# Optimization experiments

Hardware: AMD Instinct MI355X
Metric: run time of the kernel (lower is better)

The kernel has to match this reference:

```python
import jax, jax.numpy as jnp
import numpy as np
from jax import lax

BETA = 0.95
THR = 1.0
NUM_STEPS = 25
BATCH = 262144
NUM_IN, NUM_HID, NUM_OUT = 9, 100, 2


@jax.custom_vjp
def spike(u):
    # Heaviside step with ATan surrogate gradient (snntorch default, alpha=2.0)
    return (u > 0).astype(u.dtype)

def _spike_fwd(u):
    return spike(u), u

def _spike_bwd(u, g):
    return (g / (1.0 + (jnp.pi * u) ** 2),)

spike.defvjp(_spike_fwd, _spike_bwd)


def setup_inputs() -> dict:
    key = jax.random.key(0)
    k1, k2, k3, k4, k5 = jax.random.split(key, 5)
    x = jax.random.uniform(k1, (BATCH, NUM_IN), dtype=jnp.float32)
    # PyTorch-style uniform init scale ~1/sqrt(fan_in), scaled normals are fine
    W1 = jax.random.normal(k2, (NUM_HID, NUM_IN), dtype=jnp.float32) / np.sqrt(NUM_IN)
    b1 = jax.random.normal(k3, (NUM_HID,), dtype=jnp.float32) / np.sqrt(NUM_IN)
    W2 = jax.random.normal(k4, (NUM_OUT, NUM_HID), dtype=jnp.float32) / np.sqrt(NUM_HID)
    b2 = jax.random.normal(k5, (NUM_OUT,), dtype=jnp.float32) / np.sqrt(NUM_HID)
    return {"x": x, "W1": W1, "b1": b1, "W2": W2, "b2": b2}


def reference(x, W1, b1, W2, b2):
    # cur1 is identical every step (input x is static), compute once
    cur1 = x @ W1.T + b1  # [B, H]
    mem1_0 = jnp.zeros((x.shape[0], NUM_HID), dtype=x.dtype)
    mem2_0 = jnp.zeros((x.shape[0], NUM_OUT), dtype=x.dtype)

    def step(carry, _):
        mem1, mem2 = carry
        # snntorch Leaky (reset_mechanism='subtract'):
        #   reset is spike of the OLD membrane, detached from the graph
        reset1 = lax.stop_gradient(spike(mem1 - THR))
        mem1 = BETA * mem1 + cur1 - reset1 * THR
        spk1 = spike(mem1 - THR)
        cur2 = spk1 @ W2.T + b2  # [B, O]
        reset2 = lax.stop_gradient(spike(mem2 - THR))
        mem2 = BETA * mem2 + cur2 - reset2 * THR
        spk2 = spike(mem2 - THR)
        return (mem1, mem2), (spk2, mem2)

    _, (spk2_rec, mem2_rec) = lax.scan(step, (mem1_0, mem2_0), None, length=NUM_STEPS)
    return spk2_rec, mem2_rec  # each [T, B, O]
```

## Files before the change

### kernel.cpp

```cpp
#include <hip/hip_runtime.h>

#define BATCH 262144
#define NI 9
#define NH 100
#define NO 2
#define T 25


typedef float f32x2 __attribute__((ext_vector_type(2)));

#define TSTEP(t) \
  "v_pk_fma_f32 v[8:9], v[4:5], v[8:9], v[10:11]\n\t"                          \
  "v_pk_fma_f32 v[8:9], v[12:13], v[0:1], v[8:9]\n\t"                          \
  "v_pk_fma_f32 v[14:15], v[6:7], v[8:9], v[2:3]\n\t"                          \
  "v_med3_f32 v12, v14, 0, 1.0\n\t"                                            \
  "v_med3_f32 v13, v15, 0, 1.0\n\t"                                            \
  "v_pk_fma_f32 %[a" #t "], v[16:17], v[12:13], %[a" #t "] op_sel:[0,0,0] op_sel_hi:[1,0,1]\n\t" \
  "v_pk_fma_f32 %[a" #t "], v[18:19], v[12:13], %[a" #t "] op_sel:[0,1,0] op_sel_hi:[1,1,1]\n\t"

__global__
__attribute__((amdgpu_flat_work_group_size(256, 256), amdgpu_waves_per_eu(4, 8)))
void snn_fwd(
    const float* __restrict__ x,
    const float* __restrict__ W1,
    const float* __restrict__ b1,
    const float* __restrict__ W2,
    const float* __restrict__ b2,
    float* __restrict__ out)
{
    __shared__ f32x2 red[13 * 128];

    const int tid  = threadIdx.x;
    const int lane = tid & 63;
    const int w    = tid >> 6;
    const int half = __builtin_amdgcn_readfirstlane(w & 1);
    const int el   = (w >> 1) * 64 + lane;
    const int e    = blockIdx.x * 128 + el;

    float xi[NI];
#pragma unroll
    for (int i = 0; i < NI; ++i) xi[i] = x[(size_t)e * NI + i];

    f32x2 acc[T];
#pragma unroll
    for (int t = 0; t < T; ++t) { acc[t].x = 0.0f; acc[t].y = 0.0f; }

    const float* W1h = W1 + half * 50 * NI;
    const float* b1h = b1 + half * 50;
    const float* W2h = W2 + half * 50;

    asm volatile(
        "s_mov_b64 s[40:41], %[pw1]\n\t"
        "s_mov_b64 s[42:43], %[pb1]\n\t"
        "s_mov_b64 s[44:45], %[pw2]\n\t"
        "v_mov_b32 v0, 0xbf800000\n\t"
        "v_mov_b32 v1, 0xbf800000\n\t"
        "v_mov_b32 v2, 0xdd800000\n\t"
        "v_mov_b32 v3, 0xdd800000\n\t"
        "v_mov_b32 v4, 0x3f733333\n\t"
        "v_mov_b32 v5, 0x3f733333\n\t"
        "v_mov_b32 v6, 0x5d800000\n\t"
        "v_mov_b32 v7, 0x5d800000\n\t"
        "s_mov_b32 s46, 25\n\t"
        "s_load_dwordx16 s[48:63], s[40:41], 0x0\n\t"
        "s_load_dwordx2 s[64:65], s[40:41], 0x40\n\t"
        "s_load_dwordx2 s[66:67], s[42:43], 0x0\n\t"
        "s_load_dword s68, s[44:45], 0x0\n\t"
        "s_load_dword s69, s[44:45], 0x190\n\t"
        "s_load_dword s70, s[44:45], 0x4\n\t"
        "s_load_dword s71, s[44:45], 0x194\n\t"
        "1:\n\t"
        "s_waitcnt lgkmcnt(0)\n\t"
        "v_mov_b32 v16, s68\n\t"
        "v_mov_b32 v17, s69\n\t"
        "v_mov_b32 v18, s70\n\t"
        "v_mov_b32 v19, s71\n\t"
        "v_mul_f32 v10, s48, %[x0]\n\t"
        "v_fma_f32 v10, s49, %[x1], v10\n\t"
        "v_fma_f32 v10, s50, %[x2], v10\n\t"
        "v_fma_f32 v10, s51, %[x3], v10\n\t"
        "v_fma_f32 v10, s52, %[x4], v10\n\t"
        "v_fma_f32 v10, s53, %[x5], v10\n\t"
        "v_fma_f32 v10, s54, %[x6], v10\n\t"
        "v_fma_f32 v10, s55, %[x7], v10\n\t"
        "v_fma_f32 v10, s56, %[x8], v10\n\t"
        "v_add_f32 v10, s66, v10\n\t"
        "v_mul_f32 v11, s57, %[x0]\n\t"
        "v_fma_f32 v11, s58, %[x1], v11\n\t"
        "v_fma_f32 v11, s59, %[x2], v11\n\t"
        "v_fma_f32 v11, s60, %[x3], v11\n\t"
        "v_fma_f32 v11, s61, %[x4], v11\n\t"
        "v_fma_f32 v11, s62, %[x5], v11\n\t"
        "v_fma_f32 v11, s63, %[x6], v11\n\t"
        "v_fma_f32 v11, s64, %[x7], v11\n\t"
        "v_fma_f32 v11, s65, %[x8], v11\n\t"
        "v_add_f32 v11, s67, v11\n\t"
        "s_cmp_lg_u32 s46, 1\n\t"
        "s_cbranch_scc0 2f\n\t"
        "s_add_u32 s40, s40, 72\n\t"
        "s_addc_u32 s41, s41, 0\n\t"
        "s_add_u32 s42, s42, 8\n\t"
        "s_addc_u32 s43, s43, 0\n\t"
        "s_add_u32 s44, s44, 8\n\t"
        "s_addc_u32 s45, s45, 0\n\t"
        "s_load_dwordx16 s[48:63], s[40:41], 0x0\n\t"
        "s_load_dwordx2 s[64:65], s[40:41], 0x40\n\t"
        "s_load_dwordx2 s[66:67], s[42:43], 0x0\n\t"
        "s_load_dword s68, s[44:45], 0x0\n\t"
        "s_load_dword s69, s[44:45], 0x190\n\t"
        "s_load_dword s70, s[44:45], 0x4\n\t"
        "s_load_dword s71, s[44:45], 0x194\n\t"
        "2:\n\t"
        "v_max_f32 v14, v10, v11\n\t"
        "v_cmp_lt_f32 vcc, 0x3d800000, v14\n\t"
        "s_cbranch_vccz 3f\n\t"
        "v_mov_b32 v8, 0\n\t"
        "v_mov_b32 v9, 0\n\t"
        "v_mov_b32 v12, 0\n\t"
        "v_mov_b32 v13, 0\n\t"
        TSTEP(0)  TSTEP(1)  TSTEP(2)  TSTEP(3)  TSTEP(4)
        TSTEP(5)  TSTEP(6)  TSTEP(7)  TSTEP(8)  TSTEP(9)
        TSTEP(10) TSTEP(11) TSTEP(12) TSTEP(13) TSTEP(14)
        TSTEP(15) TSTEP(16) TSTEP(17) TSTEP(18) TSTEP(19)
        TSTEP(20) TSTEP(21) TSTEP(22) TSTEP(23) TSTEP(24)
        "3:\n\t"
        "s_sub_u32 s46, s46, 1\n\t"
        "s_cmp_lg_u32 s46, 0\n\t"
        "s_cbranch_scc1 1b\n\t"
        : [a0]"+v"(acc[0]),   [a1]"+v"(acc[1]),   [a2]"+v"(acc[2]),
          [a3]"+v"(acc[3]),   [a4]"+v"(acc[4]),   [a5]"+v"(acc[5]),
          [a6]"+v"(acc[6]),   [a7]"+v"(acc[7]),   [a8]"+v"(acc[8]),
          [a9]"+v"(acc[9]),   [a10]"+v"(acc[10]), [a11]"+v"(acc[11]),
          [a12]"+v"(acc[12]), [a13]"+v"(acc[13]), [a14]"+v"(acc[14]),
          [a15]"+v"(acc[15]), [a16]"+v"(acc[16]), [a17]"+v"(acc[17]),
          [a18]"+v"(acc[18]), [a19]"+v"(acc[19]), [a20]"+v"(acc[20]),
          [a21]"+v"(acc[21]), [a22]"+v"(acc[22]), [a23]"+v"(acc[23]),
          [a24]"+v"(acc[24])
        : [pw1]"s"(W1h), [pb1]"s"(b1h), [pw2]"s"(W2h),
          [x0]"v"(xi[0]), [x1]"v"(xi[1]), [x2]"v"(xi[2]), [x3]"v"(xi[3]),
          [x4]"v"(xi[4]), [x5]"v"(xi[5]), [x6]"v"(xi[6]), [x7]"v"(xi[7]),
          [x8]"v"(xi[8])
        : "s40","s41","s42","s43","s44","s45","s46","s47","s48","s49",
          "s50","s51","s52","s53","s54","s55","s56","s57","s58","s59",
          "s60","s61","s62","s63","s64","s65","s66","s67","s68","s69",
          "s70","s71",
          "v0","v1","v2","v3","v4","v5","v6","v7","v8","v9","v10","v11",
          "v12","v13","v14","v15","v16","v17","v18","v19",
          "vcc","scc","memory");

    if (half) {
#pragma unroll
        for (int t = 0; t < 13; ++t)
            red[t * 128 + el] = acc[t];
    }
    __syncthreads();
    if (!half) {
#pragma unroll
        for (int t = 0; t < 13; ++t) {
            f32x2 r = red[t * 128 + el];
            acc[t].x += r.x; acc[t].y += r.y;
        }
    }
    __syncthreads();
    if (half) {
#pragma unroll
        for (int t = 13; t < 25; ++t)
            red[(t - 13) * 128 + el] = acc[t];
    }
    __syncthreads();
    if (!half) {
#pragma unroll
        for (int t = 13; t < 25; ++t) {
            f32x2 r = red[(t - 13) * 128 + el];
            acc[t].x += r.x; acc[t].y += r.y;
        }
        const float b20 = b2[0], b21 = b2[1];
        float2* __restrict__ out_spk = (float2*)out;
        float2* __restrict__ out_mem = (float2*)(out + (size_t)T * BATCH * NO);
        float m0 = 0.0f, m1 = 0.0f, s0 = 0.0f, s1 = 0.0f;
#pragma unroll
        for (int t = 0; t < T; ++t) {
            const float c0 = acc[t].x + b20;
            const float c1 = acc[t].y + b21;
            m0 = fmaf(0.95f, m0, c0) - s0;
            m1 = fmaf(0.95f, m1, c1) - s1;
            s0 = (m0 > 1.0f) ? 1.0f : 0.0f;
            s1 = (m1 > 1.0f) ? 1.0f : 0.0f;
            out_spk[(size_t)t * BATCH + e] = make_float2(s0, s1);
            out_mem[(size_t)t * BATCH + e] = make_float2(m0, m1);
        }
    }
}

extern "C" void kernel_launch(void* const* d_in, const int* in_sizes, int n_in,
                              void* d_out, int out_size, void* d_ws, size_t ws_size,
                              hipStream_t stream) {
    const float* x  = (const float*)d_in[0];
    const float* W1 = (const float*)d_in[1];
    const float* b1 = (const float*)d_in[2];
    const float* W2 = (const float*)d_in[3];
    const float* b2 = (const float*)d_in[4];
    float* out = (float*)d_out;

    dim3 block(256);
    dim3 grid(BATCH * 2 / 256);
    snn_fwd<<<grid, block, 0, stream>>>(x, W1, b1, W2, b2, out);
}
```

Measured before the change: 180.4 us.

## Process one hidden neuron per iteration with scalar ops and per-neuron skip

Result: faster. 155.9 us (-13.6%).

```diff
diff --git a/kernel.cpp b/kernel.cpp
--- a/kernel.cpp
+++ b/kernel.cpp
@@ -7,19 +7,15 @@
 #define T 25
 
 
-typedef float f32x2 __attribute__((ext_vector_type(2)));
-
 #define TSTEP(t) \
-  "v_pk_fma_f32 v[8:9], v[4:5], v[8:9], v[10:11]\n\t"                          \
-  "v_pk_fma_f32 v[8:9], v[12:13], v[0:1], v[8:9]\n\t"                          \
-  "v_pk_fma_f32 v[14:15], v[6:7], v[8:9], v[2:3]\n\t"                          \
-  "v_med3_f32 v12, v14, 0, 1.0\n\t"                                            \
-  "v_med3_f32 v13, v15, 0, 1.0\n\t"                                            \
-  "v_pk_fma_f32 %[a" #t "], v[16:17], v[12:13], %[a" #t "] op_sel:[0,0,0] op_sel_hi:[1,0,1]\n\t" \
-  "v_pk_fma_f32 %[a" #t "], v[18:19], v[12:13], %[a" #t "] op_sel:[0,1,0] op_sel_hi:[1,1,1]\n\t"
+  "v_fma_f32 v1, v4, v1, v0\n\t" \
+  "v_fmac_f32 v1, -1.0, v2\n\t" \
+  "v_fma_f32 v2, v5, v1, -v5 clamp\n\t" \
+  "v_fmac_f32 %[a" #t "x], v6, v2\n\t" \
+  "v_fmac_f32 %[a" #t "y], v7, v2\n\t"
 
 __global__
-__attribute__((amdgpu_flat_work_group_size(256, 256), amdgpu_waves_per_eu(4, 8)))
+__attribute__((amdgpu_flat_work_group_size(256, 256), amdgpu_waves_per_eu(6, 8)))
 void snn_fwd(
     const float* __restrict__ x,
     const float* __restrict__ W1,
@@ -28,7 +24,7 @@
     const float* __restrict__ b2,
     float* __restrict__ out)
 {
-    __shared__ f32x2 red[13 * 128];
+    __shared__ float2 red[13 * 128];
 
     const int tid  = threadIdx.x;
     const int lane = tid & 63;
@@ -41,9 +37,9 @@
 #pragma unroll
     for (int i = 0; i < NI; ++i) xi[i] = x[(size_t)e * NI + i];
 
-    f32x2 acc[T];
+    float acc0[T], acc1[T];
 #pragma unroll
-    for (int t = 0; t < T; ++t) { acc[t].x = 0.0f; acc[t].y = 0.0f; }
+    for (int t = 0; t < T; ++t) { acc0[t] = 0.0f; acc1[t] = 0.0f; }
 
     const float* W1h = W1 + half * 50 * NI;
     const float* b1h = b1 + half * 50;
@@ -53,126 +49,117 @@
         "s_mov_b64 s[40:41], %[pw1]\n\t"
         "s_mov_b64 s[42:43], %[pb1]\n\t"
         "s_mov_b64 s[44:45], %[pw2]\n\t"
-        "v_mov_b32 v0, 0xbf800000\n\t"
-        "v_mov_b32 v1, 0xbf800000\n\t"
-        "v_mov_b32 v2, 0xdd800000\n\t"
-        "v_mov_b32 v3, 0xdd800000\n\t"
         "v_mov_b32 v4, 0x3f733333\n\t"
-        "v_mov_b32 v5, 0x3f733333\n\t"
-        "v_mov_b32 v6, 0x5d800000\n\t"
-        "v_mov_b32 v7, 0x5d800000\n\t"
-        "s_mov_b32 s46, 25\n\t"
-        "s_load_dwordx16 s[48:63], s[40:41], 0x0\n\t"
-        "s_load_dwordx2 s[64:65], s[40:41], 0x40\n\t"
-        "s_load_dwordx2 s[66:67], s[42:43], 0x0\n\t"
-        "s_load_dword s68, s[44:45], 0x0\n\t"
-        "s_load_dword s69, s[44:45], 0x190\n\t"
-        "s_load_dword s70, s[44:45], 0x4\n\t"
-        "s_load_dword s71, s[44:45], 0x194\n\t"
+        "v_mov_b32 v5, 0x5d800000\n\t"
+        "s_mov_b32 s62, 50\n\t"
+        "s_load_dwordx8 s[48:55], s[40:41], 0x0\n\t"
+        "s_load_dword s56, s[40:41], 0x20\n\t"
+        "s_load_dword s57, s[42:43], 0x0\n\t"
+        "s_load_dword s58, s[44:45], 0x0\n\t"
+        "s_load_dword s59, s[44:45], 0x190\n\t"
         "1:\n\t"
         "s_waitcnt lgkmcnt(0)\n\t"
-        "v_mov_b32 v16, s68\n\t"
-        "v_mov_b32 v17, s69\n\t"
-        "v_mov_b32 v18, s70\n\t"
-        "v_mov_b32 v19, s71\n\t"
-        "v_mul_f32 v10, s48, %[x0]\n\t"
-        "v_fma_f32 v10, s49, %[x1], v10\n\t"
-        "v_fma_f32 v10, s50, %[x2], v10\n\t"
-        "v_fma_f32 v10, s51, %[x3], v10\n\t"
-        "v_fma_f32 v10, s52, %[x4], v10\n\t"
-        "v_fma_f32 v10, s53, %[x5], v10\n\t"
-        "v_fma_f32 v10, s54, %[x6], v10\n\t"
-        "v_fma_f32 v10, s55, %[x7], v10\n\t"
-        "v_fma_f32 v10, s56, %[x8], v10\n\t"
-        "v_add_f32 v10, s66, v10\n\t"
-        "v_mul_f32 v11, s57, %[x0]\n\t"
-        "v_fma_f32 v11, s58, %[x1], v11\n\t"
-        "v_fma_f32 v11, s59, %[x2], v11\n\t"
-        "v_fma_f32 v11, s60, %[x3], v11\n\t"
-        "v_fma_f32 v11, s61, %[x4], v11\n\t"
-        "v_fma_f32 v11, s62, %[x5], v11\n\t"
-        "v_fma_f32 v11, s63, %[x6], v11\n\t"
-        "v_fma_f32 v11, s64, %[x7], v11\n\t"
-        "v_fma_f32 v11, s65, %[x8], v11\n\t"
-        "v_add_f32 v11, s67, v11\n\t"
-        "s_cmp_lg_u32 s46, 1\n\t"
+        "v_mov_b32 v6, s58\n\t"
+        "v_mov_b32 v7, s59\n\t"
+        "v_mul_f32 v0, s48, %[x0]\n\t"
+        "v_fma_f32 v0, s49, %[x1], v0\n\t"
+        "v_fma_f32 v0, s50, %[x2], v0\n\t"
+        "v_fma_f32 v0, s51, %[x3], v0\n\t"
+        "v_fma_f32 v0, s52, %[x4], v0\n\t"
+        "v_fma_f32 v0, s53, %[x5], v0\n\t"
+        "v_fma_f32 v0, s54, %[x6], v0\n\t"
+        "v_fma_f32 v0, s55, %[x7], v0\n\t"
+        "v_fma_f32 v0, s56, %[x8], v0\n\t"
+        "v_add_f32 v0, s57, v0\n\t"
+        "s_cmp_lg_u32 s62, 1\n\t"
         "s_cbranch_scc0 2f\n\t"
-        "s_add_u32 s40, s40, 72\n\t"
+        "s_add_u32 s40, s40, 36\n\t"
         "s_addc_u32 s41, s41, 0\n\t"
-        "s_add_u32 s42, s42, 8\n\t"
+        "s_add_u32 s42, s42, 4\n\t"
         "s_addc_u32 s43, s43, 0\n\t"
-        "s_add_u32 s44, s44, 8\n\t"
+        "s_add_u32 s44, s44, 4\n\t"
         "s_addc_u32 s45, s45, 0\n\t"
-        "s_load_dwordx16 s[48:63], s[40:41], 0x0\n\t"
-        "s_load_dwordx2 s[64:65], s[40:41], 0x40\n\t"
-        "s_load_dwordx2 s[66:67], s[42:43], 0x0\n\t"
-        "s_load_dword s68, s[44:45], 0x0\n\t"
-        "s_load_dword s69, s[44:45], 0x190\n\t"
-        "s_load_dword s70, s[44:45], 0x4\n\t"
-        "s_load_dword s71, s[44:45], 0x194\n\t"
+        "s_load_dwordx8 s[48:55], s[40:41], 0x0\n\t"
+        "s_load_dword s56, s[40:41], 0x20\n\t"
+        "s_load_dword s57, s[42:43], 0x0\n\t"
+        "s_load_dword s58, s[44:45], 0x0\n\t"
+        "s_load_dword s59, s[44:45], 0x190\n\t"
         "2:\n\t"
-        "v_max_f32 v14, v10, v11\n\t"
-        "v_cmp_lt_f32 vcc, 0x3d800000, v14\n\t"
+        "v_cmp_lt_f32 vcc, 0x3d800000, v0\n\t"
         "s_cbranch_vccz 3f\n\t"
-        "v_mov_b32 v8, 0\n\t"
-        "v_mov_b32 v9, 0\n\t"
-        "v_mov_b32 v12, 0\n\t"
-        "v_mov_b32 v13, 0\n\t"
-        TSTEP(0)  TSTEP(1)  TSTEP(2)  TSTEP(3)  TSTEP(4)
+        "v_mov_b32 v1, v0\n\t"
+        "v_fma_f32 v2, v5, v1, -v5 clamp\n\t"
+        "v_fmac_f32 %[a0x], v6, v2\n\t"
+        "v_fmac_f32 %[a0y], v7, v2\n\t"
+        TSTEP(1)  TSTEP(2)  TSTEP(3)  TSTEP(4)
         TSTEP(5)  TSTEP(6)  TSTEP(7)  TSTEP(8)  TSTEP(9)
         TSTEP(10) TSTEP(11) TSTEP(12) TSTEP(13) TSTEP(14)
         TSTEP(15) TSTEP(16) TSTEP(17) TSTEP(18) TSTEP(19)
         TSTEP(20) TSTEP(21) TSTEP(22) TSTEP(23) TSTEP(24)
         "3:\n\t"
-        "s_sub_u32 s46, s46, 1\n\t"
-        "s_cmp_lg_u32 s46, 0\n\t"
+        "s_sub_u32 s62, s62, 1\n\t"
+        "s_cmp_lg_u32 s62, 0\n\t"
         "s_cbranch_scc1 1b\n\t"
-        : [a0]"+v"(acc[0]),   [a1]"+v"(acc[1]),   [a2]"+v"(acc[2]),
-          [a3]"+v"(acc[3]),   [a4]"+v"(acc[4]),   [a5]"+v"(acc[5]),
-          [a6]"+v"(acc[6]),   [a7]"+v"(acc[7]),   [a8]"+v"(acc[8]),
-          [a9]"+v"(acc[9]),   [a10]"+v"(acc[10]), [a11]"+v"(acc[11]),
-          [a12]"+v"(acc[12]), [a13]"+v"(acc[13]), [a14]"+v"(acc[14]),
-          [a15]"+v"(acc[15]), [a16]"+v"(acc[16]), [a17]"+v"(acc[17]),
-          [a18]"+v"(acc[18]), [a19]"+v"(acc[19]), [a20]"+v"(acc[20]),
-          [a21]"+v"(acc[21]), [a22]"+v"(acc[22]), [a23]"+v"(acc[23]),
-          [a24]"+v"(acc[24])
+        : [a0x]"+v"(acc0[0]),  [a0y]"+v"(acc1[0]),
+          [a1x]"+v"(acc0[1]),  [a1y]"+v"(acc1[1]),
+          [a2x]"+v"(acc0[2]),  [a2y]"+v"(acc1[2]),
+          [a3x]"+v"(acc0[3]),  [a3y]"+v"(acc1[3]),
+          [a4x]"+v"(acc0[4]),  [a4y]"+v"(acc1[4]),
+          [a5x]"+v"(acc0[5]),  [a5y]"+v"(acc1[5]),
+          [a6x]"+v"(acc0[6]),  [a6y]"+v"(acc1[6]),
+          [a7x]"+v"(acc0[7]),  [a7y]"+v"(acc1[7]),
+          [a8x]"+v"(acc0[8]),  [a8y]"+v"(acc1[8]),
+          [a9x]"+v"(acc0[9]),  [a9y]"+v"(acc1[9]),
+          [a10x]"+v"(acc0[10]), [a10y]"+v"(acc1[10]),
+          [a11x]"+v"(acc0[11]), [a11y]"+v"(acc1[11]),
+          [a12x]"+v"(acc0[12]), [a12y]"+v"(acc1[12]),
+          [a13x]"+v"(acc0[13]), [a13y]"+v"(acc1[13]),
+          [a14x]"+v"(acc0[14]), [a14y]"+v"(acc1[14]),
+          [a15x]"+v"(acc0[15]), [a15y]"+v"(acc1[15]),
+          [a16x]"+v"(acc0[16]), [a16y]"+v"(acc1[16]),
+          [a17x]"+v"(acc0[17]), [a17y]"+v"(acc1[17]),
+          [a18x]"+v"(acc0[18]), [a18y]"+v"(acc1[18]),
+          [a19x]"+v"(acc0[19]), [a19y]"+v"(acc1[19]),
+          [a20x]"+v"(acc0[20]), [a20y]"+v"(acc1[20]),
+          [a21x]"+v"(acc0[21]), [a21y]"+v"(acc1[21]),
+          [a22x]"+v"(acc0[22]), [a22y]"+v"(acc1[22]),
+          [a23x]"+v"(acc0[23]), [a23y]"+v"(acc1[23]),
+          [a24x]"+v"(acc0[24]), [a24y]"+v"(acc1[24])
         : [pw1]"s"(W1h), [pb1]"s"(b1h), [pw2]"s"(W2h),
           [x0]"v"(xi[0]), [x1]"v"(xi[1]), [x2]"v"(xi[2]), [x3]"v"(xi[3]),
           [x4]"v"(xi[4]), [x5]"v"(xi[5]), [x6]"v"(xi[6]), [x7]"v"(xi[7]),
           [x8]"v"(xi[8])
         : "s40","s41","s42","s43","s44","s45","s46","s47","s48","s49",
           "s50","s51","s52","s53","s54","s55","s56","s57","s58","s59",
-          "s60","s61","s62","s63","s64","s65","s66","s67","s68","s69",
-          "s70","s71",
-          "v0","v1","v2","v3","v4","v5","v6","v7","v8","v9","v10","v11",
-          "v12","v13","v14","v15","v16","v17","v18","v19",
+          "s60","s61","s62",
+          "v0","v1","v2","v3","v4","v5","v6","v7",
           "vcc","scc","memory");
 
     if (half) {
 #pragma unroll
         for (int t = 0; t < 13; ++t)
-            red[t * 128 + el] = acc[t];
+            red[t * 128 + el] = make_float2(acc0[t], acc1[t]);
     }
     __syncthreads();
     if (!half) {
 #pragma unroll
         for (int t = 0; t < 13; ++t) {
-            f32x2 r = red[t * 128 + el];
-            acc[t].x += r.x; acc[t].y += r.y;
+            float2 r = red[t * 128 + el];
+            acc0[t] += r.x; acc1[t] += r.y;
         }
     }
     __syncthreads();
     if (half) {
 #pragma unroll
         for (int t = 13; t < 25; ++t)
-            red[(t - 13) * 128 + el] = acc[t];
+            red[(t - 13) * 128 + el] = make_float2(acc0[t], acc1[t]);
     }
     __syncthreads();
     if (!half) {
 #pragma unroll
         for (int t = 13; t < 25; ++t) {
-            f32x2 r = red[(t - 13) * 128 + el];
-            acc[t].x += r.x; acc[t].y += r.y;
+            float2 r = red[(t - 13) * 128 + el];
+            acc0[t] += r.x; acc1[t] += r.y;
         }
         const float b20 = b2[0], b21 = b2[1];
         float2* __restrict__ out_spk = (float2*)out;
@@ -180,8 +167,8 @@
         float m0 = 0.0f, m1 = 0.0f, s0 = 0.0f, s1 = 0.0f;
 #pragma unroll
         for (int t = 0; t < T; ++t) {
-            const float c0 = acc[t].x + b20;
-            const float c1 = acc[t].y + b21;
+            const float c0 = acc0[t] + b20;
+            const float c1 = acc1[t] + b21;
             m0 = fmaf(0.95f, m0, c0) - s0;
             m1 = fmaf(0.95f, m1, c1) - s1;
             s0 = (m0 > 1.0f) ? 1.0f : 0.0f;
```
